# Performance work log

Hardware: AMD Instinct MI355X
Metric: run time of the kernel (lower is better)

The kernel has to match this reference:

```python
import jax, jax.numpy as jnp
import numpy as np

DIM = 512   # feature channels (dim)
K = 3       # depthwise kernel size
H = 256     # grid extent along pos[:,0]
W = 256     # grid extent along pos[:,1]
N = 20000   # number of occupied spots (unique coordinates)


def setup_inputs() -> dict:
    key = jax.random.key(0)
    k1, k2, k3 = jax.random.split(key, 3)
    rng = np.random.default_rng(0)
    # N unique flat cells; pin corners so the dense grid extent is exactly HxW
    flat = np.concatenate([[0, H * W - 1], rng.permutation(H * W - 2)[: N - 2] + 1])
    pos = jnp.asarray(np.stack([flat // W, flat % W], axis=1), dtype=jnp.int32)  # (N,2)
    x = jax.random.normal(k1, (1, N, DIM), jnp.float32)
    weight = jax.random.normal(k2, (DIM, 1, K, K), jnp.float32) * 0.05  # depthwise OIHW
    bias = jax.random.normal(k3, (DIM,), jnp.float32) * 0.05
    return {"x": x, "pos": pos, "weight": weight, "bias": bias}


def reference(x, pos, weight, bias):
    pos = pos - pos.min(axis=0)                 # shift to origin (as torch)
    p0, p1 = pos[:, 0], pos[:, 1]
    xsq = x[0]                                  # (N, DIM)
    # scatter sparse coords to dense grid (duplicates would sum, coords unique)
    grid = jnp.zeros((H, W, DIM), x.dtype).at[p0, p1].add(xsq)   # (H, W, DIM)
    xd = grid.transpose(2, 1, 0)[None]          # (1, DIM, W, H) == permute(2,1,0).unsqueeze(0)
    conv = jax.lax.conv_general_dilated(
        xd, weight, (1, 1), "SAME",
        dimension_numbers=("NCHW", "OIHW", "NCHW"),
        feature_group_count=DIM,
    ) + bias[None, :, None, None]
    mask = xd.sum(axis=1, keepdims=True) != 0.0  # occupied cells
    out_d = jnp.where(mask, conv, 0.0) + xd      # masked residual
    dense = out_d[0].transpose(2, 1, 0)          # (H, W, DIM)
    # gather back to sparse values; torch to_sparse(2) orders rows lexicographically
    order = jnp.lexsort((p1, p0))
    vals = dense[p0[order], p1[order]]           # (N, DIM)
    return vals[None]                            # (1, N, DIM)
```

## Files before the change

kernel.cpp:

```cpp
#include <hip/hip_runtime.h>

#define HH 256
#define WW 256
#define DIM 512


__global__ __launch_bounds__(256) void init_kernel(int* __restrict__ cell_map,
                                                   int* __restrict__ counts) {
    int idx = blockIdx.x * 256 + threadIdx.x;
    cell_map[idx] = -1;
    if (blockIdx.x == 0) counts[threadIdx.x] = 0;
}

__global__ __launch_bounds__(256) void scatter_kernel(const int* __restrict__ pos,
                                                      int* __restrict__ cell_map,
                                                      int* __restrict__ counts,
                                                      int n) {
    int i = blockIdx.x * 256 + threadIdx.x;
    if (i >= n) return;
    int p0 = pos[2 * i];
    int p1 = pos[2 * i + 1];
    int flat = p0 * WW + p1;
    cell_map[flat] = i;
    atomicAdd(&counts[flat >> 8], 1);
}

__global__ __launch_bounds__(256) void scan_kernel(const int* __restrict__ counts,
                                                   int* __restrict__ offsets) {
    __shared__ int tmp[256];
    int t = threadIdx.x;
    int v = counts[t];
    tmp[t] = v;
    __syncthreads();
    for (int d = 1; d < 256; d <<= 1) {
        int add = (t >= d) ? tmp[t - d] : 0;
        __syncthreads();
        tmp[t] += add;
        __syncthreads();
    }
    offsets[t] = tmp[t] - v;
}

__global__ __launch_bounds__(256) void rank_kernel(const int* __restrict__ cell_map,
                                                   const int* __restrict__ offsets,
                                                   int* __restrict__ out_row) {
    __shared__ int wt[4];
    int t = threadIdx.x;
    int cell = blockIdx.x * 256 + t;
    int m = cell_map[cell];
    bool occ = (m >= 0);
    unsigned long long mask = __ballot(occ);
    int lane = t & 63;
    int wave = t >> 6;
    int pre = __popcll(mask & ((1ull << lane) - 1ull));
    if (lane == 0) wt[wave] = __popcll(mask);
    __syncthreads();
    int woff = 0;
    for (int i = 0; i < wave; ++i) woff += wt[i];
    if (occ) out_row[m] = offsets[blockIdx.x] + woff + pre;
}

__global__ __launch_bounds__(256) void conv_main(const float* __restrict__ x,
                                                 const int* __restrict__ pos,
                                                 const float* __restrict__ weight,
                                                 const float* __restrict__ bias,
                                                 const int* __restrict__ cell_map,
                                                 const int* __restrict__ out_row,
                                                 float* __restrict__ out,
                                                 int n, int ppb) {
    __shared__ float s_w[9 * DIM];
    __shared__ int s_nb[2][9];
    const int t = threadIdx.x;

    for (int i = t; i < 9 * DIM; i += 256) {
        int c = i / 9, k = i % 9;
        s_w[k * DIM + c] = weight[i];
    }

    const int c0 = 2 * t;
    const float2 bia = *(const float2*)(bias + c0);

    int base = blockIdx.x * ppb;
    int end  = base + ppb;
    if (end > n) end = n;

    int buf = 0;
    for (int p = base; p < end; ++p, buf ^= 1) {
        if (t < 9) {
            int dh = t % 3 - 1;
            int dw = t / 3 - 1;
            int p0 = pos[2 * p] + dh;
            int p1 = pos[2 * p + 1] + dw;
            s_nb[buf][t] = (p0 >= 0 && p0 < HH && p1 >= 0 && p1 < WW)
                               ? cell_map[p0 * WW + p1] : -1;
        }
        __syncthreads();

        float2 xv = *(const float2*)(x + (size_t)p * DIM + c0);
        float acc0 = xv.x + bia.x;
        float acc1 = xv.y + bia.y;

        #pragma unroll
        for (int k = 0; k < 9; ++k) {
            int m = s_nb[buf][k];
            if (m >= 0) {
                float2 xn = *(const float2*)(x + (size_t)m * DIM + c0);
                float2 wv = *(const float2*)(s_w + k * DIM + c0);
                acc0 += xn.x * wv.x;
                acc1 += xn.y * wv.y;
            }
        }

        int r = out_row[p];
        float2 res; res.x = acc0; res.y = acc1;
        *(float2*)(out + (size_t)r * DIM + c0) = res;
    }
}

extern "C" void kernel_launch(void* const* d_in, const int* in_sizes, int n_in,
                              void* d_out, int out_size, void* d_ws, size_t ws_size,
                              hipStream_t stream) {
    const float* x      = (const float*)d_in[0];
    const int*   pos    = (const int*)d_in[1];
    const float* weight = (const float*)d_in[2];
    const float* bias   = (const float*)d_in[3];
    float* out = (float*)d_out;

    int n = in_sizes[1] / 2;

    int* ws       = (int*)d_ws;
    int* cell_map = ws;
    int* counts   = ws + HH * WW;
    int* offsets  = ws + HH * WW + 256;
    int* out_row  = ws + HH * WW + 512;

    init_kernel<<<256, 256, 0, stream>>>(cell_map, counts);
    scatter_kernel<<<(n + 255) / 256, 256, 0, stream>>>(pos, cell_map, counts, n);
    scan_kernel<<<1, 256, 0, stream>>>(counts, offsets);
    rank_kernel<<<256, 256, 0, stream>>>(cell_map, offsets, out_row);

    const int nblocks = 2000;
    int ppb = (n + nblocks - 1) / nblocks;
    conv_main<<<nblocks, 256, 0, stream>>>(x, pos, weight, bias, cell_map,
                                           out_row, out, n, ppb);
}
```

Baseline: 134.5 us.

## Restructure conv to one wave per output row with register weights

Merges the scan into the rank kernel, which now writes a sorted list of packed (input index, cell) entries, and replaces the init kernel with memsets. The conv kernel now assigns one wavefront per output row in sorted order. Each lane handles 8 channels with float4 loads, holds its weights and bias in registers, and folds the residual into the centre tap. Neighbour lookups move from a shared-memory stage behind a block barrier to per-wave direct cell_map reads, and outputs use nontemporal stores. The aim is to remove the per-point __syncthreads, the extra kernel launches and the scattered output writes, at the cost of higher register pressure and packing limits on the index and cell (16 bits each).

Result: faster. 127.3 us (-5.3%).

```diff
diff --git a/kernel.cpp b/kernel.cpp
--- a/kernel.cpp
+++ b/kernel.cpp
@@ -4,13 +4,8 @@
 #define WW 256
 #define DIM 512
 
+typedef float f32x4 __attribute__((ext_vector_type(4)));
 
-__global__ __launch_bounds__(256) void init_kernel(int* __restrict__ cell_map,
-                                                   int* __restrict__ counts) {
-    int idx = blockIdx.x * 256 + threadIdx.x;
-    cell_map[idx] = -1;
-    if (blockIdx.x == 0) counts[threadIdx.x] = 0;
-}
 
 __global__ __launch_bounds__(256) void scatter_kernel(const int* __restrict__ pos,
                                                       int* __restrict__ cell_map,
@@ -25,12 +20,14 @@
     atomicAdd(&counts[flat >> 8], 1);
 }
 
-__global__ __launch_bounds__(256) void scan_kernel(const int* __restrict__ counts,
-                                                   int* __restrict__ offsets) {
+__global__ __launch_bounds__(256) void rank_kernel(const int* __restrict__ cell_map,
+                                                   const int* __restrict__ counts,
+                                                   int* __restrict__ sorted) {
     __shared__ int tmp[256];
+    __shared__ int wt[4];
     int t = threadIdx.x;
-    int v = counts[t];
-    tmp[t] = v;
+    int b = blockIdx.x;
+    tmp[t] = counts[t];
     __syncthreads();
     for (int d = 1; d < 256; d <<= 1) {
         int add = (t >= d) ? tmp[t - d] : 0;
@@ -38,15 +35,9 @@
         tmp[t] += add;
         __syncthreads();
     }
-    offsets[t] = tmp[t] - v;
-}
+    int blk_off = (b > 0) ? tmp[b - 1] : 0;
 
-__global__ __launch_bounds__(256) void rank_kernel(const int* __restrict__ cell_map,
-                                                   const int* __restrict__ offsets,
-                                                   int* __restrict__ out_row) {
-    __shared__ int wt[4];
-    int t = threadIdx.x;
-    int cell = blockIdx.x * 256 + t;
+    int cell = b * 256 + t;
     int m = cell_map[cell];
     bool occ = (m >= 0);
     unsigned long long mask = __ballot(occ);
@@ -57,63 +48,87 @@
     __syncthreads();
     int woff = 0;
     for (int i = 0; i < wave; ++i) woff += wt[i];
-    if (occ) out_row[m] = offsets[blockIdx.x] + woff + pre;
+    if (occ) sorted[blk_off + woff + pre] = (m << 16) | cell;
 }
 
 __global__ __launch_bounds__(256) void conv_main(const float* __restrict__ x,
-                                                 const int* __restrict__ pos,
                                                  const float* __restrict__ weight,
                                                  const float* __restrict__ bias,
                                                  const int* __restrict__ cell_map,
-                                                 const int* __restrict__ out_row,
+                                                 const int* __restrict__ sorted,
                                                  float* __restrict__ out,
-                                                 int n, int ppb) {
-    __shared__ float s_w[9 * DIM];
-    __shared__ int s_nb[2][9];
-    const int t = threadIdx.x;
+                                                 int n) {
+    const int lane = threadIdx.x & 63;
+    const int wv   = threadIdx.x >> 6;
+    const int c0   = lane * 8;
 
-    for (int i = t; i < 9 * DIM; i += 256) {
-        int c = i / 9, k = i % 9;
-        s_w[k * DIM + c] = weight[i];
+    float wt[72];
+    {
+        const float4* wb = (const float4*)(weight + c0 * 9);
+        #pragma unroll
+        for (int q = 0; q < 18; ++q) {
+            float4 v = wb[q];
+            wt[4 * q + 0] = v.x; wt[4 * q + 1] = v.y;
+            wt[4 * q + 2] = v.z; wt[4 * q + 3] = v.w;
+        }
     }
+    float bj[8];
+    {
+        float4 b0 = *(const float4*)(bias + c0);
+        float4 b1 = *(const float4*)(bias + c0 + 4);
+        bj[0]=b0.x; bj[1]=b0.y; bj[2]=b0.z; bj[3]=b0.w;
+        bj[4]=b1.x; bj[5]=b1.y; bj[6]=b1.z; bj[7]=b1.w;
+    }
+    #pragma unroll
+    for (int j = 0; j < 8; ++j) wt[j * 9 + 4] += 1.0f;
 
-    const int c0 = 2 * t;
-    const float2 bia = *(const float2*)(bias + c0);
+    int ppb  = (n + gridDim.x - 1) / gridDim.x;
+    int base = blockIdx.x * ppb;
+    int endr = base + ppb; if (endr > n) endr = n;
 
-    int base = blockIdx.x * ppb;
-    int end  = base + ppb;
-    if (end > n) end = n;
+    for (int r = base + wv; r < endr; r += 4) {
+        int packed = sorted[r];
+        packed = __builtin_amdgcn_readfirstlane(packed);
+        int p    = packed >> 16;
+        int flat = packed & 0xFFFF;
+        int h = flat >> 8;
+        int w = flat & (WW - 1);
 
-    int buf = 0;
-    for (int p = base; p < end; ++p, buf ^= 1) {
-        if (t < 9) {
-            int dh = t % 3 - 1;
-            int dw = t / 3 - 1;
-            int p0 = pos[2 * p] + dh;
-            int p1 = pos[2 * p + 1] + dw;
-            s_nb[buf][t] = (p0 >= 0 && p0 < HH && p1 >= 0 && p1 < WW)
-                               ? cell_map[p0 * WW + p1] : -1;
-        }
-        __syncthreads();
-
-        float2 xv = *(const float2*)(x + (size_t)p * DIM + c0);
-        float acc0 = xv.x + bia.x;
-        float acc1 = xv.y + bia.y;
+        const float* xs = x + (size_t)p * DIM + c0;
+        float4 s0 = *(const float4*)(xs);
+        float4 s1 = *(const float4*)(xs + 4);
+        float acc[8];
+        acc[0] = bj[0] + s0.x * wt[0*9+4]; acc[1] = bj[1] + s0.y * wt[1*9+4];
+        acc[2] = bj[2] + s0.z * wt[2*9+4]; acc[3] = bj[3] + s0.w * wt[3*9+4];
+        acc[4] = bj[4] + s1.x * wt[4*9+4]; acc[5] = bj[5] + s1.y * wt[5*9+4];
+        acc[6] = bj[6] + s1.z * wt[6*9+4]; acc[7] = bj[7] + s1.w * wt[7*9+4];
 
         #pragma unroll
         for (int k = 0; k < 9; ++k) {
-            int m = s_nb[buf][k];
+            if (k == 4) continue;
+            int dh = k % 3 - 1;
+            int dw = k / 3 - 1;
+            int hh = h + dh;
+            int ww = w + dw;
+            int m = -1;
+            if ((unsigned)hh < (unsigned)HH && (unsigned)ww < (unsigned)WW)
+                m = cell_map[hh * WW + ww];
             if (m >= 0) {
-                float2 xn = *(const float2*)(x + (size_t)m * DIM + c0);
-                float2 wv = *(const float2*)(s_w + k * DIM + c0);
-                acc0 += xn.x * wv.x;
-                acc1 += xn.y * wv.y;
+                const float* xn = x + (size_t)m * DIM + c0;
+                float4 n0 = *(const float4*)(xn);
+                float4 n1 = *(const float4*)(xn + 4);
+                acc[0] += n0.x * wt[0*9+k]; acc[1] += n0.y * wt[1*9+k];
+                acc[2] += n0.z * wt[2*9+k]; acc[3] += n0.w * wt[3*9+k];
+                acc[4] += n1.x * wt[4*9+k]; acc[5] += n1.y * wt[5*9+k];
+                acc[6] += n1.z * wt[6*9+k]; acc[7] += n1.w * wt[7*9+k];
             }
         }
 
-        int r = out_row[p];
-        float2 res; res.x = acc0; res.y = acc1;
-        *(float2*)(out + (size_t)r * DIM + c0) = res;
+        float* op = out + (size_t)r * DIM + c0;
+        f32x4 o0 = { acc[0], acc[1], acc[2], acc[3] };
+        f32x4 o1 = { acc[4], acc[5], acc[6], acc[7] };
+        __builtin_nontemporal_store(o0, (f32x4*)op);
+        __builtin_nontemporal_store(o1, (f32x4*)(op + 4));
     }
 }
 
@@ -131,16 +146,14 @@
     int* ws       = (int*)d_ws;
     int* cell_map = ws;
     int* counts   = ws + HH * WW;
-    int* offsets  = ws + HH * WW + 256;
-    int* out_row  = ws + HH * WW + 512;
+    int* sorted   = ws + HH * WW + 256;
 
-    init_kernel<<<256, 256, 0, stream>>>(cell_map, counts);
+    (void)hipMemsetAsync(cell_map, 0xFF, HH * WW * sizeof(int), stream);
+    (void)hipMemsetAsync(counts, 0, 256 * sizeof(int), stream);
+
     scatter_kernel<<<(n + 255) / 256, 256, 0, stream>>>(pos, cell_map, counts, n);
-    scan_kernel<<<1, 256, 0, stream>>>(counts, offsets);
-    rank_kernel<<<256, 256, 0, stream>>>(cell_map, offsets, out_row);
+    rank_kernel<<<256, 256, 0, stream>>>(cell_map, counts, sorted);
 
-    const int nblocks = 2000;
-    int ppb = (n + nblocks - 1) / nblocks;
-    conv_main<<<nblocks, 256, 0, stream>>>(x, pos, weight, bias, cell_map,
-                                           out_row, out, n, ppb);
+    const int nblocks = 1024;
+    conv_main<<<nblocks, 256, 0, stream>>>(x, weight, bias, cell_map, sorted, out, n);
 }
```
